# Kernel tuning notes

Hardware: AMD Instinct MI355X
Metric: run time of the kernel (lower is better)

Reference implementation:

```python
import jax, jax.numpy as jnp
import numpy as np

B, IN, OUT = 256, 1024, 1024
P = 0.5  # drop probability


def setup_inputs() -> dict:
    key = jax.random.key(0)
    k1, k2, k3, k4, k5 = jax.random.split(key, 5)
    bound = 1.0 / np.sqrt(IN)
    inputs = {
        "input": jax.random.normal(k1, (B, IN), dtype=jnp.float32),
        "weight": jax.random.uniform(k2, (OUT, IN), dtype=jnp.float32, minval=-bound, maxval=bound),
        "bias": jax.random.uniform(k3, (OUT,), dtype=jnp.float32, minval=-bound, maxval=bound),
        # mask==True means the weight/bias element is dropped (masked_fill to 0)
        "weight_mask": jax.random.bernoulli(k4, P, (B, OUT, IN)),
        "bias_mask": jax.random.bernoulli(k5, P, (B, OUT)),
    }
    return inputs


def reference(input, weight, bias, weight_mask, bias_mask):
    # drop_connect_training:
    # y[b,o] = sum_i x[b,i] * (0 if weight_mask[b,o,i] else weight[o,i])
    keep = (~weight_mask).astype(weight.dtype)  # [B, OUT, IN]
    y = jnp.einsum("bi,oi,boi->bo", input, weight, keep)
    # bias with per-sample bias mask
    y = y + jnp.where(bias_mask, jnp.zeros((), dtype=bias.dtype), bias)
    return y
```

## Files before the change

kernel.cpp:

```cpp
#include <hip/hip_runtime.h>


#define B_   256
#define IN_  1024
#define OUT_ 1024

__global__ __launch_bounds__(256) void dropconnect_kernel(
    const float* __restrict__ x,
    const float* __restrict__ w,
    const float* __restrict__ bias,
    const int*   __restrict__ wmask,
    const int*   __restrict__ bmask,
    float*       __restrict__ out)
{
    const int wave = blockIdx.x * (blockDim.x >> 6) + (threadIdx.x >> 6);
    const int lane = threadIdx.x & 63;
    const int b = wave >> 10;
    const int o = wave & 1023;

    const float4* xr = reinterpret_cast<const float4*>(x + (size_t)b * IN_);
    const float4* wr = reinterpret_cast<const float4*>(w + (size_t)o * IN_);
    const int4*   mr = reinterpret_cast<const int4*>(wmask + (size_t)wave * IN_);

    float acc = 0.0f;
    #pragma unroll
    for (int c = 0; c < 4; ++c) {
        const int idx = c * 64 + lane;
        const float4 xv = xr[idx];
        const float4 wv = wr[idx];
        const int4   mv = mr[idx];
        acc += (mv.x == 0) ? xv.x * wv.x : 0.0f;
        acc += (mv.y == 0) ? xv.y * wv.y : 0.0f;
        acc += (mv.z == 0) ? xv.z * wv.z : 0.0f;
        acc += (mv.w == 0) ? xv.w * wv.w : 0.0f;
    }

    #pragma unroll
    for (int off = 32; off > 0; off >>= 1)
        acc += __shfl_down(acc, off, 64);

    if (lane == 0) {
        const float bv = (bmask[wave] != 0) ? 0.0f : bias[o];
        out[wave] = acc + bv;
    }
}

extern "C" void kernel_launch(void* const* d_in, const int* in_sizes, int n_in,
                              void* d_out, int out_size, void* d_ws, size_t ws_size,
                              hipStream_t stream) {
    const float* x     = (const float*)d_in[0];
    const float* w     = (const float*)d_in[1];
    const float* bias  = (const float*)d_in[2];
    const int*   wmask = (const int*)d_in[3];
    const int*   bmask = (const int*)d_in[4];
    float* out = (float*)d_out;

    const int total_waves = B_ * OUT_;
    const int waves_per_block = 256 / 64;
    const int blocks = total_waves / waves_per_block;

    dropconnect_kernel<<<blocks, 256, 0, stream>>>(x, w, bias, wmask, bmask, out);
}
```

Measured before the change: 219.7 us.

## Process two batch rows per wave to reuse weight loads, nontemporal mask loads

Each wave now computes two batch rows for the same output, so each weight row load serves two mask rows and the wave count is halved. Mask loads use nontemporal hints so the 1 GB streaming mask does not pollute the caches. Multiple accumulators with FMA and xor shuffles shorten the dependency chains. The kernel is dominated by mask bandwidth, so the gain is likely limited to fewer weight fetches and lower scheduling overhead.

After: 193.8 us. -11.8%, faster.

```diff
diff --git a/kernel.cpp b/kernel.cpp
--- a/kernel.cpp
+++ b/kernel.cpp
@@ -4,6 +4,9 @@
 #define B_   256
 #define IN_  1024
 #define OUT_ 1024
+
+typedef int   v4i __attribute__((ext_vector_type(4)));
+typedef float v4f __attribute__((ext_vector_type(4)));
 
 __global__ __launch_bounds__(256) void dropconnect_kernel(
     const float* __restrict__ x,
@@ -13,35 +16,56 @@
     const int*   __restrict__ bmask,
     float*       __restrict__ out)
 {
-    const int wave = blockIdx.x * (blockDim.x >> 6) + (threadIdx.x >> 6);
+    const int wid  = blockIdx.x * (blockDim.x >> 6) + (threadIdx.x >> 6);
     const int lane = threadIdx.x & 63;
-    const int b = wave >> 10;
-    const int o = wave & 1023;
+    const int bh = wid >> 10;
+    const int o  = wid & 1023;
+    const int b0 = bh << 1;
 
-    const float4* xr = reinterpret_cast<const float4*>(x + (size_t)b * IN_);
-    const float4* wr = reinterpret_cast<const float4*>(w + (size_t)o * IN_);
-    const int4*   mr = reinterpret_cast<const int4*>(wmask + (size_t)wave * IN_);
+    const v4f* xr0 = reinterpret_cast<const v4f*>(x + (size_t)b0 * IN_);
+    const v4f* xr1 = reinterpret_cast<const v4f*>(x + (size_t)(b0 + 1) * IN_);
+    const v4f* wr  = reinterpret_cast<const v4f*>(w + (size_t)o * IN_);
+    const v4i* mr0 = reinterpret_cast<const v4i*>(wmask + ((size_t)b0 * OUT_ + o) * IN_);
+    const v4i* mr1 = reinterpret_cast<const v4i*>(wmask + ((size_t)(b0 + 1) * OUT_ + o) * IN_);
 
-    float acc = 0.0f;
+    float a0a = 0.f, a0b = 0.f;
+    float a1a = 0.f, a1b = 0.f;
+
     #pragma unroll
     for (int c = 0; c < 4; ++c) {
         const int idx = c * 64 + lane;
-        const float4 xv = xr[idx];
-        const float4 wv = wr[idx];
-        const int4   mv = mr[idx];
-        acc += (mv.x == 0) ? xv.x * wv.x : 0.0f;
-        acc += (mv.y == 0) ? xv.y * wv.y : 0.0f;
-        acc += (mv.z == 0) ? xv.z * wv.z : 0.0f;
-        acc += (mv.w == 0) ? xv.w * wv.w : 0.0f;
+        const v4f wv = wr[idx];
+        const v4f x0 = xr0[idx];
+        const v4f x1 = xr1[idx];
+        const v4i m0 = __builtin_nontemporal_load(mr0 + idx);
+        const v4i m1 = __builtin_nontemporal_load(mr1 + idx);
+
+        a0a = fmaf(x0[0], (m0[0] == 0) ? wv[0] : 0.f, a0a);
+        a0b = fmaf(x0[1], (m0[1] == 0) ? wv[1] : 0.f, a0b);
+        a0a = fmaf(x0[2], (m0[2] == 0) ? wv[2] : 0.f, a0a);
+        a0b = fmaf(x0[3], (m0[3] == 0) ? wv[3] : 0.f, a0b);
+
+        a1a = fmaf(x1[0], (m1[0] == 0) ? wv[0] : 0.f, a1a);
+        a1b = fmaf(x1[1], (m1[1] == 0) ? wv[1] : 0.f, a1b);
+        a1a = fmaf(x1[2], (m1[2] == 0) ? wv[2] : 0.f, a1a);
+        a1b = fmaf(x1[3], (m1[3] == 0) ? wv[3] : 0.f, a1b);
     }
 
+    float a0 = a0a + a0b;
+    float a1 = a1a + a1b;
+
     #pragma unroll
-    for (int off = 32; off > 0; off >>= 1)
-        acc += __shfl_down(acc, off, 64);
+    for (int off = 32; off > 0; off >>= 1) {
+        a0 += __shfl_xor(a0, off, 64);
+        a1 += __shfl_xor(a1, off, 64);
+    }
 
     if (lane == 0) {
-        const float bv = (bmask[wave] != 0) ? 0.0f : bias[o];
-        out[wave] = acc + bv;
+        const float bv = bias[o];
+        const size_t e0 = (size_t)b0 * OUT_ + o;
+        const size_t e1 = e0 + OUT_;
+        out[e0] = a0 + ((bmask[e0] != 0) ? 0.f : bv);
+        out[e1] = a1 + ((bmask[e1] != 0) ? 0.f : bv);
     }
 }
 
@@ -55,7 +79,7 @@
     const int*   bmask = (const int*)d_in[4];
     float* out = (float*)d_out;
 
-    const int total_waves = B_ * OUT_;
+    const int total_waves = (B_ / 2) * OUT_;
     const int waves_per_block = 256 / 64;
     const int blocks = total_waves / waves_per_block;
 
```

## Process eight batch rows per wave with nontemporal mask loads

Applied to the files above, without the earlier changes.

Each wave now computes eight batch rows for one output neuron instead of one, so each weight row load is reused eight times and more independent loads are in flight per wave. Mask loads use nontemporal hints so the one-pass mask stream does not pollute the cache, and the reduction uses xor shuffles across the eight accumulators. The kernel is dominated by the 1 GiB mask stream, so reuse of weights matters little. The change adds register pressure and launches eight times fewer waves.

New measurement: 178.9 us. 18.6% less time.

```diff
diff --git a/kernel.cpp b/kernel.cpp
--- a/kernel.cpp
+++ b/kernel.cpp
@@ -4,6 +4,10 @@
 #define B_   256
 #define IN_  1024
 #define OUT_ 1024
+#define NB   8
+
+typedef int   v4i __attribute__((ext_vector_type(4)));
+typedef float v4f __attribute__((ext_vector_type(4)));
 
 __global__ __launch_bounds__(256) void dropconnect_kernel(
     const float* __restrict__ x,
@@ -13,35 +17,61 @@
     const int*   __restrict__ bmask,
     float*       __restrict__ out)
 {
-    const int wave = blockIdx.x * (blockDim.x >> 6) + (threadIdx.x >> 6);
+    const int wid  = blockIdx.x * (blockDim.x >> 6) + (threadIdx.x >> 6);
     const int lane = threadIdx.x & 63;
-    const int b = wave >> 10;
-    const int o = wave & 1023;
+    const int bg = wid >> 10;
+    const int o  = wid & 1023;
+    const int b0 = bg * NB;
 
-    const float4* xr = reinterpret_cast<const float4*>(x + (size_t)b * IN_);
-    const float4* wr = reinterpret_cast<const float4*>(w + (size_t)o * IN_);
-    const int4*   mr = reinterpret_cast<const int4*>(wmask + (size_t)wave * IN_);
+    const v4f* wr = reinterpret_cast<const v4f*>(w + (size_t)o * IN_);
 
-    float acc = 0.0f;
+    const v4f* xr[NB];
+    const v4i* mr[NB];
+    #pragma unroll
+    for (int r = 0; r < NB; ++r) {
+        xr[r] = reinterpret_cast<const v4f*>(x + (size_t)(b0 + r) * IN_);
+        mr[r] = reinterpret_cast<const v4i*>(wmask + ((size_t)(b0 + r) * OUT_ + o) * IN_);
+    }
+
+    float acc[NB];
+    #pragma unroll
+    for (int r = 0; r < NB; ++r) acc[r] = 0.f;
+
     #pragma unroll
     for (int c = 0; c < 4; ++c) {
         const int idx = c * 64 + lane;
-        const float4 xv = xr[idx];
-        const float4 wv = wr[idx];
-        const int4   mv = mr[idx];
-        acc += (mv.x == 0) ? xv.x * wv.x : 0.0f;
-        acc += (mv.y == 0) ? xv.y * wv.y : 0.0f;
-        acc += (mv.z == 0) ? xv.z * wv.z : 0.0f;
-        acc += (mv.w == 0) ? xv.w * wv.w : 0.0f;
+        const v4f wv = wr[idx];
+        v4i m[NB];
+        v4f xv[NB];
+        #pragma unroll
+        for (int r = 0; r < NB; ++r) {
+            m[r]  = __builtin_nontemporal_load(mr[r] + idx);
+            xv[r] = xr[r][idx];
+        }
+        #pragma unroll
+        for (int r = 0; r < NB; ++r) {
+            acc[r] = fmaf(xv[r][0], (m[r][0] == 0) ? wv[0] : 0.f, acc[r]);
+            acc[r] = fmaf(xv[r][1], (m[r][1] == 0) ? wv[1] : 0.f, acc[r]);
+            acc[r] = fmaf(xv[r][2], (m[r][2] == 0) ? wv[2] : 0.f, acc[r]);
+            acc[r] = fmaf(xv[r][3], (m[r][3] == 0) ? wv[3] : 0.f, acc[r]);
+        }
     }
 
     #pragma unroll
-    for (int off = 32; off > 0; off >>= 1)
-        acc += __shfl_down(acc, off, 64);
+    for (int off = 32; off > 0; off >>= 1) {
+        #pragma unroll
+        for (int r = 0; r < NB; ++r)
+            acc[r] += __shfl_xor(acc[r], off, 64);
+    }
 
     if (lane == 0) {
-        const float bv = (bmask[wave] != 0) ? 0.0f : bias[o];
-        out[wave] = acc + bv;
+        const float bv = bias[o];
+        const size_t e0 = (size_t)b0 * OUT_ + o;
+        #pragma unroll
+        for (int r = 0; r < NB; ++r) {
+            const size_t e = e0 + (size_t)r * OUT_;
+            out[e] = acc[r] + ((bmask[e] != 0) ? 0.f : bv);
+        }
     }
 }
 
@@ -55,7 +85,7 @@
     const int*   bmask = (const int*)d_in[4];
     float* out = (float*)d_out;
 
-    const int total_waves = B_ * OUT_;
+    const int total_waves = (B_ / NB) * OUT_;
     const int waves_per_block = 256 / 64;
     const int blocks = total_waves / waves_per_block;
 
```
